# Optimization experiments

Measured on AMD Instinct MI355X. Metric: run time of the kernel, lower is better.

The kernel has to match this reference:

```python
import jax, jax.numpy as jnp
import numpy as np
import math

BLUR = [1.0, 3.0, 3.0, 1.0]
FACTOR = 2


def make_kernel():
    k = jnp.array(BLUR, dtype=jnp.float32)
    k = k[None, :] * k[:, None]
    k = k / k.sum()
    return k * (FACTOR ** 2)  # Upsample scales kernel by factor**2


def setup_inputs() -> dict:
    key = jax.random.key(0)
    k1, k2, k3 = jax.random.split(key, 3)
    B, C, H, W = 8, 512, 128, 128
    inp = jax.random.normal(k1, (B, C, H, W), dtype=jnp.float32)
    skip = jax.random.normal(k2, (B, 3, H // 2, W // 2), dtype=jnp.float32)
    weight = jax.random.normal(k3, (3, C, 3, 3), dtype=jnp.float32)  # EqualConv2d raw weight
    bias = jnp.zeros((3,), dtype=jnp.float32)
    return {"input": inp, "skip": skip, "weight": weight, "bias": bias}


def _upfirdn2d_up2(x, kernel):
    # upfirdn2d(x, kernel, up=2, down=1, pad=(pad0, pad1)) as in StyleGAN2.
    # Zero-stuffing by `factor` then pad (pad0, pad1) then VALID conv with
    # flipped kernel == lax conv with lhs_dilation=factor and right pad
    # extended by (factor-1) (trailing zeros of the stuffed signal).
    kh = kernel.shape[0]
    p = kh - FACTOR
    pad0 = (p + 1) // 2 + FACTOR - 1  # = 2 for k=4, factor=2
    pad1 = p // 2                      # = 1
    C = x.shape[1]
    w = jnp.flip(kernel, (0, 1))[None, None]        # [1,1,kh,kw] (conv, not corr)
    w = jnp.tile(w, (C, 1, 1, 1))                   # depthwise [C,1,kh,kw]
    pad = (pad0, pad1 + FACTOR - 1)
    return jax.lax.conv_general_dilated(
        x, w, window_strides=(1, 1), padding=(pad, pad),
        lhs_dilation=(FACTOR, FACTOR), feature_group_count=C,
        dimension_numbers=("NCHW", "OIHW", "NCHW"))


def reference(input, skip, weight, bias):
    C = input.shape[1]
    scale = 1.0 / math.sqrt(C * 3 * 3)  # equalized-lr scale
    out = jax.lax.conv_general_dilated(
        input, weight * scale, window_strides=(1, 1), padding=((1, 1), (1, 1)),
        dimension_numbers=("NCHW", "OIHW", "NCHW"))
    out = out + bias[None, :, None, None]
    out = out + _upfirdn2d_up2(skip, make_kernel())
    return out
```

## Files before the change

kernel.cpp:

```cpp
#include <hip/hip_runtime.h>
#include <math.h>

#define BATCH 8
#define CIN 512
#define H 128
#define W 128
#define COUT 3
#define CHUNKS 32
#define CH (CIN / CHUNKS)
#define R 8
#define NROWS (R + 2)
#define WAVES 4
#define BLOCK_ROWS (R * WAVES)
#define TILES_Y (H / BLOCK_ROWS)

__device__ __forceinline__ void compute_ch(
    const float2 (&cur)[NROWS], const float* __restrict__ wp,
    float (&acc)[R][2][3], int lane, float m0, float m9)
{
    float wv[27];
#pragma unroll
    for (int co = 0; co < 3; co++)
#pragma unroll
        for (int k = 0; k < 9; k++)
            wv[co * 9 + k] = wp[co * (CIN * 9) + k];

    float lw[3], ax[3], ay[3], rw[3];
#pragma unroll
    for (int rr = 0; rr < NROWS; rr++) {
        const int s = rr % 3;
        float vx = cur[rr].x, vy = cur[rr].y;
        if (rr == 0)         { vx *= m0; vy *= m0; }
        if (rr == NROWS - 1) { vx *= m9; vy *= m9; }
        float l = __shfl_up(vy, 1);
        float r_ = __shfl_down(vx, 1);
        lw[s] = (lane == 0)  ? 0.f : l;
        rw[s] = (lane == 63) ? 0.f : r_;
        ax[s] = vx; ay[s] = vy;

        if (rr >= 2) {
            const int p  = rr - 2;
            const int s0 = p % 3, s1 = (p + 1) % 3, s2 = (p + 2) % 3;
#pragma unroll
            for (int co = 0; co < 3; co++) {
                const float* w = &wv[co * 9];
                float a0 = acc[p][0][co], a1 = acc[p][1][co];
                a0 += lw[s0] * w[0] + ax[s0] * w[1] + ay[s0] * w[2];
                a1 += ax[s0] * w[0] + ay[s0] * w[1] + rw[s0] * w[2];
                a0 += lw[s1] * w[3] + ax[s1] * w[4] + ay[s1] * w[5];
                a1 += ax[s1] * w[3] + ay[s1] * w[4] + rw[s1] * w[5];
                a0 += lw[s2] * w[6] + ax[s2] * w[7] + ay[s2] * w[8];
                a1 += ax[s2] * w[6] + ay[s2] * w[7] + rw[s2] * w[8];
                acc[p][0][co] = a0; acc[p][1][co] = a1;
            }
        }
    }
}

__device__ __forceinline__ void prefetch_ch(
    float2 (&buf)[NROWS], const float* __restrict__ chan,
    const int (&goff)[NROWS], int x0)
{
#pragma unroll
    for (int r = 0; r < NROWS; r++)
        buf[r] = *(const float2*)(chan + goff[r] + x0);
}

__global__ __launch_bounds__(256) void torgb_conv(
    const float* __restrict__ in, const float* __restrict__ skip,
    const float* __restrict__ weight, const float* __restrict__ bias,
    float* __restrict__ out)
{
    const int bx    = blockIdx.x;
    const int tile  = bx & (TILES_Y - 1);
    const int b     = (bx >> 2) & (BATCH - 1);
    const int chunk = bx >> 5;
    const int ci0   = chunk * CH;

    const int tid  = threadIdx.x;
    const int lane = tid & 63;
    const int wave = tid >> 6;
    const int yb   = tile * BLOCK_ROWS + wave * R;
    const int x0   = 2 * lane;

    int goff[NROWS];
#pragma unroll
    for (int r = 0; r < NROWS; r++) {
        int g = yb - 1 + r;
        int gc = g < 0 ? 0 : (g > H - 1 ? H - 1 : g);
        goff[r] = gc * W;
    }
    const float m0 = (yb >= 1) ? 1.f : 0.f;
    const float m9 = (yb + R <= H - 1) ? 1.f : 0.f;

    float acc[R][2][3];
#pragma unroll
    for (int p = 0; p < R; p++)
#pragma unroll
        for (int q = 0; q < 2; q++)
#pragma unroll
            for (int c = 0; c < 3; c++) acc[p][q][c] = 0.f;

    const float* chan0 = in + ((size_t)b * CIN + ci0) * H * W;
    const float* wbase = weight + (size_t)ci0 * 9;

    float2 bufA[NROWS], bufB[NROWS];
    prefetch_ch(bufA, chan0, goff, x0);

#pragma unroll 2
    for (int ci = 0; ci < CH; ci += 2) {
        prefetch_ch(bufB, chan0 + (size_t)(ci + 1) * H * W, goff, x0);
        compute_ch(bufA, wbase + (size_t)ci * 9, acc, lane, m0, m9);
        if (ci + 2 < CH)
            prefetch_ch(bufA, chan0 + (size_t)(ci + 2) * H * W, goff, x0);
        compute_ch(bufB, wbase + (size_t)(ci + 1) * 9, acc, lane, m0, m9);
    }

    const float scale = 1.0f / sqrtf((float)(CIN * 9));
    float* outb = out + (size_t)b * COUT * H * W;

    int j0[2], j1[2]; float wh0[2], wh1[2]; bool j0ok[2], j1ok[2];
#pragma unroll
    for (int q = 0; q < 2; q++) {
        int x = x0 + q;
        if ((x & 1) == 0) { j0[q] = x >> 1;       wh0[q] = 0.75f; j1[q] = (x >> 1) - 1; wh1[q] = 0.25f; }
        else              { j0[q] = (x + 1) >> 1; wh0[q] = 0.25f; j1[q] = (x - 1) >> 1; wh1[q] = 0.75f; }
        j0ok[q] = (j0[q] >= 0 && j0[q] < 64);
        j1ok[q] = (j1[q] >= 0 && j1[q] < 64);
    }

#pragma unroll
    for (int p = 0; p < R; p++) {
        int y = yb + p;
        int i0, i1; float wv0, wv1;
        if ((y & 1) == 0) { i0 = y >> 1;       wv0 = 0.75f; i1 = (y >> 1) - 1; wv1 = 0.25f; }
        else              { i0 = (y + 1) >> 1; wv0 = 0.25f; i1 = (y - 1) >> 1; wv1 = 0.75f; }
        const bool i0ok = (i0 >= 0 && i0 < 64), i1ok = (i1 >= 0 && i1 < 64);
#pragma unroll
        for (int q = 0; q < 2; q++) {
            int x = x0 + q;
#pragma unroll
            for (int co = 0; co < 3; co++) {
                float v = acc[p][q][co] * scale;
                if (chunk == 0) {
                    const float* sk = skip + (size_t)(b * COUT + co) * 64 * 64;
                    float s00 = (i0ok && j0ok[q]) ? sk[i0 * 64 + j0[q]] : 0.f;
                    float s01 = (i0ok && j1ok[q]) ? sk[i0 * 64 + j1[q]] : 0.f;
                    float s10 = (i1ok && j0ok[q]) ? sk[i1 * 64 + j0[q]] : 0.f;
                    float s11 = (i1ok && j1ok[q]) ? sk[i1 * 64 + j1[q]] : 0.f;
                    v += bias[co] + wv0 * (wh0[q] * s00 + wh1[q] * s01)
                                  + wv1 * (wh0[q] * s10 + wh1[q] * s11);
                }
                atomicAdd(&outb[(size_t)co * H * W + y * W + x], v);
            }
        }
    }
}

extern "C" void kernel_launch(void* const* d_in, const int* in_sizes, int n_in,
                              void* d_out, int out_size, void* d_ws, size_t ws_size,
                              hipStream_t stream) {
    const float* in     = (const float*)d_in[0];
    const float* skip   = (const float*)d_in[1];
    const float* weight = (const float*)d_in[2];
    const float* bias   = (const float*)d_in[3];
    float* out = (float*)d_out;

    hipMemsetAsync(out, 0, (size_t)out_size * sizeof(float), stream);
    dim3 grid(CHUNKS * BATCH * TILES_Y);
    torgb_conv<<<grid, 256, 0, stream>>>(in, skip, weight, bias, out);
}
```

Measured before the change: 432.1 us.

## Replace atomic accumulation with workspace partials plus reduce kernel, one column per lane

Each lane now computes a single output column instead of two adjacent ones, so global loads are coalesced scalar loads and the halo columns at wave edges are fetched with an extra per-lane load and a shuffle. Blocks cover 16 rows by two 64-column halves. Channel chunks drop from 32 to 16. When the workspace is large enough, partial sums go to a per-chunk workspace without atomics, and a second kernel sums the chunks and adds the upsampled skip and bias. This removes the memset and the atomic traffic, at the cost of extra workspace writes and reads and a second kernel launch.

Measured after the change: 490.9 us. 1.14x slower.

```diff
diff --git a/kernel.cpp b/kernel.cpp
--- a/kernel.cpp
+++ b/kernel.cpp
@@ -6,17 +6,27 @@
 #define H 128
 #define W 128
 #define COUT 3
-#define CHUNKS 32
+#define CHUNKS 16
 #define CH (CIN / CHUNKS)
 #define R 8
 #define NROWS (R + 2)
-#define WAVES 4
-#define BLOCK_ROWS (R * WAVES)
+#define BLOCK_ROWS 16
 #define TILES_Y (H / BLOCK_ROWS)
+#define HWP (H * W)
+
+__device__ __forceinline__ void pf(float (&v)[NROWS], float& hp,
+                                   const float* __restrict__ chan,
+                                   const int (&goff)[NROWS], int colOff, int hoff)
+{
+#pragma unroll
+    for (int r = 0; r < NROWS; r++)
+        v[r] = chan[goff[r] + colOff];
+    hp = chan[hoff];
+}
 
 __device__ __forceinline__ void compute_ch(
-    const float2 (&cur)[NROWS], const float* __restrict__ wp,
-    float (&acc)[R][2][3], int lane, float m0, float m9)
+    const float (&v)[NROWS], float hp, const float* __restrict__ wp,
+    float (&acc)[R * 3], int lane, float m0, float m9, float lex, float rex)
 {
     float wv[27];
 #pragma unroll
@@ -25,18 +35,19 @@
         for (int k = 0; k < 9; k++)
             wv[co * 9 + k] = wp[co * (CIN * 9) + k];
 
-    float lw[3], ax[3], ay[3], rw[3];
+    float wl[3], wm[3], wr[3];
 #pragma unroll
     for (int rr = 0; rr < NROWS; rr++) {
         const int s = rr % 3;
-        float vx = cur[rr].x, vy = cur[rr].y;
-        if (rr == 0)         { vx *= m0; vy *= m0; }
-        if (rr == NROWS - 1) { vx *= m9; vy *= m9; }
-        float l = __shfl_up(vy, 1);
-        float r_ = __shfl_down(vx, 1);
-        lw[s] = (lane == 0)  ? 0.f : l;
-        rw[s] = (lane == 63) ? 0.f : r_;
-        ax[s] = vx; ay[s] = vy;
+        float mrow = (rr == 0) ? m0 : ((rr == NROWS - 1) ? m9 : 1.f);
+        float mv = v[rr] * mrow;
+        float hL = __shfl(hp, 2 * rr)     * (mrow * lex);
+        float hR = __shfl(hp, 2 * rr + 1) * (mrow * rex);
+        float lf = __shfl_up(mv, 1);
+        float rg = __shfl_down(mv, 1);
+        wl[s] = (lane == 0)  ? hL : lf;
+        wm[s] = mv;
+        wr[s] = (lane == 63) ? hR : rg;
 
         if (rr >= 2) {
             const int p  = rr - 2;
@@ -44,44 +55,36 @@
 #pragma unroll
             for (int co = 0; co < 3; co++) {
                 const float* w = &wv[co * 9];
-                float a0 = acc[p][0][co], a1 = acc[p][1][co];
-                a0 += lw[s0] * w[0] + ax[s0] * w[1] + ay[s0] * w[2];
-                a1 += ax[s0] * w[0] + ay[s0] * w[1] + rw[s0] * w[2];
-                a0 += lw[s1] * w[3] + ax[s1] * w[4] + ay[s1] * w[5];
-                a1 += ax[s1] * w[3] + ay[s1] * w[4] + rw[s1] * w[5];
-                a0 += lw[s2] * w[6] + ax[s2] * w[7] + ay[s2] * w[8];
-                a1 += ax[s2] * w[6] + ay[s2] * w[7] + rw[s2] * w[8];
-                acc[p][0][co] = a0; acc[p][1][co] = a1;
+                float a = acc[p * 3 + co];
+                a += wl[s0] * w[0] + wm[s0] * w[1] + wr[s0] * w[2];
+                a += wl[s1] * w[3] + wm[s1] * w[4] + wr[s1] * w[5];
+                a += wl[s2] * w[6] + wm[s2] * w[7] + wr[s2] * w[8];
+                acc[p * 3 + co] = a;
             }
         }
     }
 }
 
-__device__ __forceinline__ void prefetch_ch(
-    float2 (&buf)[NROWS], const float* __restrict__ chan,
-    const int (&goff)[NROWS], int x0)
-{
-#pragma unroll
-    for (int r = 0; r < NROWS; r++)
-        buf[r] = *(const float2*)(chan + goff[r] + x0);
-}
-
+template <bool USE_WS>
 __global__ __launch_bounds__(256) void torgb_conv(
     const float* __restrict__ in, const float* __restrict__ skip,
     const float* __restrict__ weight, const float* __restrict__ bias,
-    float* __restrict__ out)
+    float* __restrict__ out, float* __restrict__ ws)
 {
     const int bx    = blockIdx.x;
     const int tile  = bx & (TILES_Y - 1);
-    const int b     = (bx >> 2) & (BATCH - 1);
-    const int chunk = bx >> 5;
+    const int b     = (bx >> 3) & (BATCH - 1);
+    const int chunk = bx >> 6;
     const int ci0   = chunk * CH;
 
     const int tid  = threadIdx.x;
     const int lane = tid & 63;
     const int wave = tid >> 6;
-    const int yb   = tile * BLOCK_ROWS + wave * R;
-    const int x0   = 2 * lane;
+    const int rs   = wave >> 1;
+    const int chq  = wave & 1;
+    const int cw   = chq * 64;
+    const int yb   = tile * BLOCK_ROWS + rs * R;
+    const int colOff = cw + lane;
 
     int goff[NROWS];
 #pragma unroll
@@ -90,71 +93,126 @@
         int gc = g < 0 ? 0 : (g > H - 1 ? H - 1 : g);
         goff[r] = gc * W;
     }
-    const float m0 = (yb >= 1) ? 1.f : 0.f;
-    const float m9 = (yb + R <= H - 1) ? 1.f : 0.f;
-
-    float acc[R][2][3];
-#pragma unroll
-    for (int p = 0; p < R; p++)
-#pragma unroll
-        for (int q = 0; q < 2; q++)
-#pragma unroll
-            for (int c = 0; c < 3; c++) acc[p][q][c] = 0.f;
-
-    const float* chan0 = in + ((size_t)b * CIN + ci0) * H * W;
+    const float m0  = (yb >= 1) ? 1.f : 0.f;
+    const float m9  = (yb + R <= H - 1) ? 1.f : 0.f;
+    const float lex = (cw > 0) ? 1.f : 0.f;
+    const float rex = (cw + 64 < W) ? 1.f : 0.f;
+
+    int hoff;
+    {
+        int rr = lane >> 1; if (rr > NROWS - 1) rr = NROWS - 1;
+        int side = lane & 1;
+        int g = yb - 1 + rr; g = g < 0 ? 0 : (g > H - 1 ? H - 1 : g);
+        int hcol = cw - 1 + 65 * side;
+        hcol = hcol < 0 ? 0 : (hcol > W - 1 ? W - 1 : hcol);
+        hoff = g * W + hcol;
+    }
+
+    float acc[R * 3];
+#pragma unroll
+    for (int i = 0; i < R * 3; i++) acc[i] = 0.f;
+
+    const float* chan0 = in + ((size_t)b * CIN + ci0) * HWP;
     const float* wbase = weight + (size_t)ci0 * 9;
 
-    float2 bufA[NROWS], bufB[NROWS];
-    prefetch_ch(bufA, chan0, goff, x0);
+    float vA[NROWS], vB[NROWS], hA, hB;
+    pf(vA, hA, chan0, goff, colOff, hoff);
 
 #pragma unroll 2
     for (int ci = 0; ci < CH; ci += 2) {
-        prefetch_ch(bufB, chan0 + (size_t)(ci + 1) * H * W, goff, x0);
-        compute_ch(bufA, wbase + (size_t)ci * 9, acc, lane, m0, m9);
+        pf(vB, hB, chan0 + (size_t)(ci + 1) * HWP, goff, colOff, hoff);
+        compute_ch(vA, hA, wbase + (size_t)ci * 9, acc, lane, m0, m9, lex, rex);
         if (ci + 2 < CH)
-            prefetch_ch(bufA, chan0 + (size_t)(ci + 2) * H * W, goff, x0);
-        compute_ch(bufB, wbase + (size_t)(ci + 1) * 9, acc, lane, m0, m9);
+            pf(vA, hA, chan0 + (size_t)(ci + 2) * HWP, goff, colOff, hoff);
+        compute_ch(vB, hB, wbase + (size_t)(ci + 1) * 9, acc, lane, m0, m9, lex, rex);
     }
 
     const float scale = 1.0f / sqrtf((float)(CIN * 9));
-    float* outb = out + (size_t)b * COUT * H * W;
-
-    int j0[2], j1[2]; float wh0[2], wh1[2]; bool j0ok[2], j1ok[2];
-#pragma unroll
-    for (int q = 0; q < 2; q++) {
-        int x = x0 + q;
-        if ((x & 1) == 0) { j0[q] = x >> 1;       wh0[q] = 0.75f; j1[q] = (x >> 1) - 1; wh1[q] = 0.25f; }
-        else              { j0[q] = (x + 1) >> 1; wh0[q] = 0.25f; j1[q] = (x - 1) >> 1; wh1[q] = 0.75f; }
-        j0ok[q] = (j0[q] >= 0 && j0[q] < 64);
-        j1ok[q] = (j1[q] >= 0 && j1[q] < 64);
-    }
-
-#pragma unroll
-    for (int p = 0; p < R; p++) {
-        int y = yb + p;
-        int i0, i1; float wv0, wv1;
-        if ((y & 1) == 0) { i0 = y >> 1;       wv0 = 0.75f; i1 = (y >> 1) - 1; wv1 = 0.25f; }
-        else              { i0 = (y + 1) >> 1; wv0 = 0.25f; i1 = (y - 1) >> 1; wv1 = 0.75f; }
-        const bool i0ok = (i0 >= 0 && i0 < 64), i1ok = (i1 >= 0 && i1 < 64);
-#pragma unroll
-        for (int q = 0; q < 2; q++) {
-            int x = x0 + q;
+
+    if (USE_WS) {
+        float* dst = ws + (((size_t)chunk * BATCH + b) * COUT) * HWP;
+#pragma unroll
+        for (int p = 0; p < R; p++) {
+            int y = yb + p;
+#pragma unroll
+            for (int co = 0; co < 3; co++)
+                dst[(size_t)co * HWP + y * W + colOff] = acc[p * 3 + co] * scale;
+        }
+    } else {
+        float* outb = out + (size_t)b * COUT * HWP;
+        const int x = colOff;
+        int j0, j1; float wh0, wh1;
+        if ((x & 1) == 0) { j0 = x >> 1;       wh0 = 0.75f; j1 = (x >> 1) - 1; wh1 = 0.25f; }
+        else              { j0 = (x + 1) >> 1; wh0 = 0.25f; j1 = (x - 1) >> 1; wh1 = 0.75f; }
+        const bool j0ok = (j0 >= 0 && j0 < 64), j1ok = (j1 >= 0 && j1 < 64);
+#pragma unroll
+        for (int p = 0; p < R; p++) {
+            int y = yb + p;
+            int i0, i1; float wv0, wv1;
+            if ((y & 1) == 0) { i0 = y >> 1;       wv0 = 0.75f; i1 = (y >> 1) - 1; wv1 = 0.25f; }
+            else              { i0 = (y + 1) >> 1; wv0 = 0.25f; i1 = (y - 1) >> 1; wv1 = 0.75f; }
+            const bool i0ok = (i0 >= 0 && i0 < 64), i1ok = (i1 >= 0 && i1 < 64);
 #pragma unroll
             for (int co = 0; co < 3; co++) {
-                float v = acc[p][q][co] * scale;
+                float vv = acc[p * 3 + co] * scale;
                 if (chunk == 0) {
                     const float* sk = skip + (size_t)(b * COUT + co) * 64 * 64;
-                    float s00 = (i0ok && j0ok[q]) ? sk[i0 * 64 + j0[q]] : 0.f;
-                    float s01 = (i0ok && j1ok[q]) ? sk[i0 * 64 + j1[q]] : 0.f;
-                    float s10 = (i1ok && j0ok[q]) ? sk[i1 * 64 + j0[q]] : 0.f;
-                    float s11 = (i1ok && j1ok[q]) ? sk[i1 * 64 + j1[q]] : 0.f;
-                    v += bias[co] + wv0 * (wh0[q] * s00 + wh1[q] * s01)
-                                  + wv1 * (wh0[q] * s10 + wh1[q] * s11);
+                    float s00 = (i0ok && j0ok) ? sk[i0 * 64 + j0] : 0.f;
+                    float s01 = (i0ok && j1ok) ? sk[i0 * 64 + j1] : 0.f;
+                    float s10 = (i1ok && j0ok) ? sk[i1 * 64 + j0] : 0.f;
+                    float s11 = (i1ok && j1ok) ? sk[i1 * 64 + j1] : 0.f;
+                    vv += bias[co] + wv0 * (wh0 * s00 + wh1 * s01)
+                                   + wv1 * (wh0 * s10 + wh1 * s11);
                 }
-                atomicAdd(&outb[(size_t)co * H * W + y * W + x], v);
+                atomicAdd(&outb[(size_t)co * HWP + y * W + x], vv);
             }
         }
     }
+}
+
+__global__ __launch_bounds__(256) void torgb_reduce(
+    const float* __restrict__ ws, const float* __restrict__ skip,
+    const float* __restrict__ bias, float* __restrict__ out)
+{
+    const int n4 = BATCH * COUT * HWP / 4;
+    int e4 = blockIdx.x * 256 + threadIdx.x;
+    if (e4 >= n4) return;
+
+    const int x4  = e4 & (W / 4 - 1);
+    const int y   = (e4 >> 5) & (H - 1);
+    const int co  = (e4 >> 12) % COUT;
+    const int b   = e4 / (COUT * H * W / 4);
+    const int x0  = x4 * 4;
+
+    float4 sum = make_float4(0.f, 0.f, 0.f, 0.f);
+#pragma unroll
+    for (int c = 0; c < CHUNKS; c++) {
+        const float4 v = *(const float4*)&ws[((((size_t)c * BATCH + b) * COUT + co) * H + y) * W + x0];
+        sum.x += v.x; sum.y += v.y; sum.z += v.z; sum.w += v.w;
+    }
+
+    int i0, i1; float wv0, wv1;
+    if ((y & 1) == 0) { i0 = y >> 1;       wv0 = 0.75f; i1 = (y >> 1) - 1; wv1 = 0.25f; }
+    else              { i0 = (y + 1) >> 1; wv0 = 0.25f; i1 = (y - 1) >> 1; wv1 = 0.75f; }
+    const bool i0ok = (i0 >= 0 && i0 < 64), i1ok = (i1 >= 0 && i1 < 64);
+    const float* sk = skip + (size_t)(b * COUT + co) * 64 * 64;
+    const float bi = bias[co];
+
+    float r[4] = {sum.x, sum.y, sum.z, sum.w};
+#pragma unroll
+    for (int q = 0; q < 4; q++) {
+        int x = x0 + q;
+        int j0, j1; float wh0, wh1;
+        if ((x & 1) == 0) { j0 = x >> 1;       wh0 = 0.75f; j1 = (x >> 1) - 1; wh1 = 0.25f; }
+        else              { j0 = (x + 1) >> 1; wh0 = 0.25f; j1 = (x - 1) >> 1; wh1 = 0.75f; }
+        const bool j0ok = (j0 >= 0 && j0 < 64), j1ok = (j1 >= 0 && j1 < 64);
+        float s00 = (i0ok && j0ok) ? sk[i0 * 64 + j0] : 0.f;
+        float s01 = (i0ok && j1ok) ? sk[i0 * 64 + j1] : 0.f;
+        float s10 = (i1ok && j0ok) ? sk[i1 * 64 + j0] : 0.f;
+        float s11 = (i1ok && j1ok) ? sk[i1 * 64 + j1] : 0.f;
+        r[q] += bi + wv0 * (wh0 * s00 + wh1 * s01) + wv1 * (wh0 * s10 + wh1 * s11);
+    }
+    *(float4*)&out[(size_t)e4 * 4] = make_float4(r[0], r[1], r[2], r[3]);
 }
 
 extern "C" void kernel_launch(void* const* d_in, const int* in_sizes, int n_in,
@@ -165,8 +223,17 @@
     const float* weight = (const float*)d_in[2];
     const float* bias   = (const float*)d_in[3];
     float* out = (float*)d_out;
-
-    hipMemsetAsync(out, 0, (size_t)out_size * sizeof(float), stream);
-    dim3 grid(CHUNKS * BATCH * TILES_Y);
-    torgb_conv<<<grid, 256, 0, stream>>>(in, skip, weight, bias, out);
-}
+    float* ws  = (float*)d_ws;
+
+    const size_t ws_needed = (size_t)CHUNKS * BATCH * COUT * HWP * sizeof(float);
+    const dim3 grid(CHUNKS * BATCH * TILES_Y);
+
+    if (ws_size >= ws_needed) {
+        torgb_conv<true><<<grid, 256, 0, stream>>>(in, skip, weight, bias, out, ws);
+        const int n4 = BATCH * COUT * HWP / 4;
+        torgb_reduce<<<(n4 + 255) / 256, 256, 0, stream>>>(ws, skip, bias, out);
+    } else {
+        hipMemsetAsync(out, 0, (size_t)out_size * sizeof(float), stream);
+        torgb_conv<false><<<grid, 256, 0, stream>>>(in, skip, weight, bias, out, ws);
+    }
+}
```
